# Kernel tuning notes

Measured on AMD Instinct MI355X. Metric: run time of the kernel, lower is better.

## Reference

```python
import jax, jax.numpy as jnp
import numpy as np

N = 100000      # nodes
E = 1600000     # edges
F_IN = 16       # in_features
H = 64          # hidden_channels (heads=1)
E_DIM = 9       # edge_dim
NEG_SLOPE = 0.2


def setup_inputs() -> dict:
    key = jax.random.key(0)
    ks = jax.random.split(key, 11)
    x = jax.random.normal(ks[0], (N, F_IN), jnp.float32)
    edge_index = jax.random.randint(ks[1], (2, E), 0, N, dtype=jnp.int64)
    edge_attr = jax.random.normal(ks[2], (E, E_DIM), jnp.float32)
    s_in = 1.0 / np.sqrt(F_IN)
    s_e = 1.0 / np.sqrt(E_DIM)
    s_h = 1.0 / np.sqrt(H)
    W = jax.random.uniform(ks[3], (F_IN, H), jnp.float32, -s_in, s_in)        # GATConv.lin
    W_edge = jax.random.uniform(ks[4], (E_DIM, H), jnp.float32, -s_e, s_e)    # GATConv.lin_edge
    att_src = jax.random.normal(ks[5], (H,), jnp.float32) * 0.1
    att_dst = jax.random.normal(ks[6], (H,), jnp.float32) * 0.1
    att_edge = jax.random.normal(ks[7], (H,), jnp.float32) * 0.1
    bias = jnp.zeros((H,), jnp.float32)                                        # GATConv bias
    lin_w = jax.random.uniform(ks[8], (H, 1), jnp.float32, -s_h, s_h)          # self.lin
    lin_b = jnp.zeros((1,), jnp.float32)
    return {"x": x, "edge_attr": edge_attr, "W": W, "W_edge": W_edge,
            "att_src": att_src, "att_dst": att_dst, "att_edge": att_edge,
            "bias": bias, "lin_w": lin_w, "lin_b": lin_b, "edge_index": edge_index}


def _gat_forward(x, edge_attr, W, W_edge, att_src, att_dst, att_edge, bias,
                 lin_w, lin_b, edge_index):
    n = x.shape[0]
    src, dst = edge_index[0], edge_index[1]
    h = x @ W                                   # [N, H]
    a_src = h @ att_src                         # [N]
    a_dst = h @ att_dst                         # [N]
    # add_self_loops with fill_value='mean': per-node mean of incoming edge_attr
    ones = jnp.ones((src.shape[0],), x.dtype)
    deg = jax.ops.segment_sum(ones, dst, num_segments=n)
    loop_attr = jax.ops.segment_sum(edge_attr, dst, num_segments=n) / jnp.maximum(deg, 1.0)[:, None]
    loops = jnp.arange(n, dtype=src.dtype)
    src_f = jnp.concatenate([src, loops])       # [E+N]
    dst_f = jnp.concatenate([dst, loops])
    ea_f = jnp.concatenate([edge_attr, loop_attr], axis=0)
    a_edge = (ea_f @ W_edge) @ att_edge         # [E+N]
    alpha = a_src[src_f] + a_dst[dst_f] + a_edge
    alpha = jnp.where(alpha >= 0, alpha, NEG_SLOPE * alpha)  # leaky_relu
    # segment softmax over destination nodes (every node has a self-loop -> no empty segments)
    amax = jax.ops.segment_max(alpha, dst_f, num_segments=n)
    ex = jnp.exp(alpha - amax[dst_f])
    denom = jax.ops.segment_sum(ex, dst_f, num_segments=n)
    alpha = ex / (denom[dst_f] + 1e-16)
    msg = h[src_f] * alpha[:, None]             # [E+N, H]
    out_nodes = jax.ops.segment_sum(msg, dst_f, num_segments=n) + bias
    x2 = jax.nn.relu(out_nodes)
    # edge readout on the ORIGINAL edge list
    pair = (x2[src] + x2[dst]) * 0.5            # [E, H]
    return jax.nn.sigmoid(pair @ lin_w + lin_b) # [E, 1]


def reference(x, edge_attr, W, W_edge, att_src, att_dst, att_edge, bias,
              lin_w, lin_b, edge_index):
    return _gat_forward(x, edge_attr, W, W_edge, att_src, att_dst, att_edge,
                        bias, lin_w, lin_b, edge_index)
```

## Files before the change

kernel.cpp:

```cpp
#include <hip/hip_runtime.h>
#include <hip/hip_bf16.h>
#include <hip/hip_fp16.h>
#include <math.h>

#define N_NODES 100000
#define N_EDGES 1600000
#define F_IN 16
#define HDIM 64
#define E_DIM 9
#define NEG 0.2f

#define CAP 64
#define NSLICE 8
#define SLICE_W 12500
#define SLICE_CAP 210000
#define PART_BLOCKS 1024
#define FIXSCALE 16777216.0f
#define GPAD 64

typedef unsigned long long ull;
typedef long long ll;

__global__ __launch_bounds__(256) void k_node_h(
    const float* __restrict__ x, const float* __restrict__ W,
    const float* __restrict__ att_src, const float* __restrict__ att_dst,
    __hip_bfloat16* __restrict__ hbf, float* __restrict__ a_src,
    float* __restrict__ a_dst) {
  __shared__ float sW[F_IN * HDIM];
  int t = threadIdx.x;
  for (int i = t; i < F_IN * HDIM; i += 256) sW[i] = W[i];
  __syncthreads();
  int lane = t & 63;
  int node = blockIdx.x * 4 + (t >> 6);
  if (node >= N_NODES) return;
  const float* xr = x + node * F_IN;
  float acc = 0.f;
#pragma unroll
  for (int k = 0; k < F_IN; ++k) acc += xr[k] * sW[k * HDIM + lane];
  hbf[(size_t)node * HDIM + lane] = __float2bfloat16(acc);
  float v1 = acc * att_src[lane];
  float v2 = acc * att_dst[lane];
#pragma unroll
  for (int off = 32; off > 0; off >>= 1) {
    v1 += __shfl_down(v1, off);
    v2 += __shfl_down(v2, off);
  }
  if (lane == 0) { a_src[node] = v1; a_dst[node] = v2; }
}

__global__ void k_we(const float* __restrict__ W_edge,
                     const float* __restrict__ att_edge, float* __restrict__ w_e) {
  int d = threadIdx.x;
  if (d < E_DIM) {
    float s = 0.f;
    for (int hh = 0; hh < HDIM; ++hh) s += W_edge[d * HDIM + hh] * att_edge[hh];
    w_e[d] = s;
  }
}

__global__ __launch_bounds__(256) void k_edge_pre(
    const float* __restrict__ ea, const int* __restrict__ ei,
    const float* __restrict__ w_e, const float* __restrict__ a_src,
    const float* __restrict__ a_dst, ull* __restrict__ sstream,
    unsigned* __restrict__ gcount) {
  __shared__ float sea[256 * E_DIM];
  __shared__ float swe[E_DIM];
  __shared__ unsigned wcnt[4][NSLICE];
  __shared__ unsigned woff[4][NSLICE];
  __shared__ unsigned gbase[NSLICE];
  int t = threadIdx.x;
  int wave = t >> 6, lane = t & 63;
  if (t < E_DIM) swe[t] = w_e[t];
  size_t tile = (size_t)blockIdx.x * (256 * E_DIM);
#pragma unroll
  for (int i = 0; i < E_DIM; ++i)
    sea[i * 256 + t] = __builtin_nontemporal_load(ea + tile + i * 256 + t);
  int e = blockIdx.x * 256 + t;
  int s = __builtin_nontemporal_load(ei + e);
  int d = __builtin_nontemporal_load(ei + N_EDGES + e);
  __syncthreads();
  float a_e = 0.f;
#pragma unroll
  for (int k = 0; k < E_DIM; ++k) a_e += sea[t * E_DIM + k] * swe[k];
  float al = a_src[s] + a_dst[d] + a_e;
  al = al >= 0.f ? al : NEG * al;
  float ee = expf(al);
  unsigned b = __float_as_uint(ee);
  b += 0x7fffu + ((b >> 16) & 1u);
  unsigned pk = ((unsigned)s << 15) | ((b >> 16) & 0x7fffu);
  unsigned slice = (unsigned)d / SLICE_W;
  unsigned dloc = (unsigned)d - slice * SLICE_W;
  unsigned aeh = (unsigned)__half_as_ushort(__float2half(a_e));
  ull entry = ((ull)dloc << 48) | ((ull)aeh << 32) | (ull)pk;
  ull lt = (lane == 63) ? 0x7FFFFFFFFFFFFFFFull : ((1ull << lane) - 1ull);
  unsigned myrank = 0;
#pragma unroll
  for (int si = 0; si < NSLICE; ++si) {
    ull m = __ballot(slice == (unsigned)si);
    if (slice == (unsigned)si) myrank = (unsigned)__popcll(m & lt);
    if (lane == 0) wcnt[wave][si] = (unsigned)__popcll(m);
  }
  __syncthreads();
  if (t < NSLICE) {
    unsigned a = 0;
#pragma unroll
    for (int w = 0; w < 4; ++w) { woff[w][t] = a; a += wcnt[w][t]; }
    gbase[t] = atomicAdd(gcount + t * GPAD, a);
  }
  __syncthreads();
  unsigned off = gbase[slice] + woff[wave][slice] + myrank;
  if (off < SLICE_CAP)
    __builtin_nontemporal_store(entry, sstream + (size_t)slice * SLICE_CAP + off);
}

__global__ __launch_bounds__(256) void k_part2(
    const ull* __restrict__ sstream, const unsigned* __restrict__ gcount,
    ull* __restrict__ packed, unsigned* __restrict__ bpack) {
  int t = threadIdx.x;
  int slice = blockIdx.x & (NSLICE - 1);
  int j = blockIdx.x >> 3;
  unsigned n = gcount[slice * GPAD];
  const ull* sp = sstream + (size_t)slice * SLICE_CAP;
  int lo = slice * SLICE_W;
  const unsigned stride = (PART_BLOCKS / NSLICE) * 256;
  for (unsigned i = (unsigned)j * 256 + t; i < n; i += stride) {
    ull entry = sp[i];
    int d = lo + (int)(unsigned)(entry >> 48);
    float ae = __half2float(__ushort_as_half((unsigned short)((entry >> 32) & 0xFFFFu)));
    unsigned pk = (unsigned)(entry & 0xFFFFFFFFu);
    ll q = (ll)lrintf(ae * FIXSCALE);
    ull old = atomicAdd(packed + d, ((ull)q << 20) | 1ull);
    unsigned pos = (unsigned)(old & 0xFFFFFu);
    if (pos < CAP) bpack[(size_t)d * CAP + pos] = pk;
  }
}

__global__ __launch_bounds__(256) void k_gather(
    const ull* __restrict__ packed, const unsigned* __restrict__ bpack,
    const __hip_bfloat16* __restrict__ hbf, const float* __restrict__ a_src,
    const float* __restrict__ a_dst, const float* __restrict__ bias,
    const float* __restrict__ lin_w, float* __restrict__ s_node) {
  int t = threadIdx.x;
  int lane = t & 63;
  int node = blockIdx.x * 4 + (t >> 6);
  if (node >= N_NODES) return;
  ull p = packed[node];
  unsigned deg = (unsigned)(p & 0xFFFFFu);
  float sumae = (float)((double)((ll)p >> 20) * (1.0 / (double)FIXSCALE));
  const unsigned* row = bpack + (size_t)node * CAP;
  float acc = 0.f, denom = 0.f;
  unsigned k = 0;
  for (; k + 8 <= deg; k += 8) {
    uint4 pa = *(const uint4*)(row + k);
    uint4 pb = *(const uint4*)(row + k + 4);
    float e0 = __uint_as_float((pa.x & 0x7fffu) << 16);
    float e1 = __uint_as_float((pa.y & 0x7fffu) << 16);
    float e2 = __uint_as_float((pa.z & 0x7fffu) << 16);
    float e3 = __uint_as_float((pa.w & 0x7fffu) << 16);
    float e4 = __uint_as_float((pb.x & 0x7fffu) << 16);
    float e5 = __uint_as_float((pb.y & 0x7fffu) << 16);
    float e6 = __uint_as_float((pb.z & 0x7fffu) << 16);
    float e7 = __uint_as_float((pb.w & 0x7fffu) << 16);
    float h0 = __bfloat162float(hbf[(size_t)(pa.x >> 15) * HDIM + lane]);
    float h1 = __bfloat162float(hbf[(size_t)(pa.y >> 15) * HDIM + lane]);
    float h2 = __bfloat162float(hbf[(size_t)(pa.z >> 15) * HDIM + lane]);
    float h3 = __bfloat162float(hbf[(size_t)(pa.w >> 15) * HDIM + lane]);
    float h4 = __bfloat162float(hbf[(size_t)(pb.x >> 15) * HDIM + lane]);
    float h5 = __bfloat162float(hbf[(size_t)(pb.y >> 15) * HDIM + lane]);
    float h6 = __bfloat162float(hbf[(size_t)(pb.z >> 15) * HDIM + lane]);
    float h7 = __bfloat162float(hbf[(size_t)(pb.w >> 15) * HDIM + lane]);
    denom += ((e0 + e1) + (e2 + e3)) + ((e4 + e5) + (e6 + e7));
    acc += (e0 * h0 + e1 * h1 + e2 * h2 + e3 * h3)
         + (e4 * h4 + e5 * h5 + e6 * h6 + e7 * h7);
  }
  for (; k + 4 <= deg; k += 4) {
    uint4 p4 = *(const uint4*)(row + k);
    float e0 = __uint_as_float((p4.x & 0x7fffu) << 16);
    float e1 = __uint_as_float((p4.y & 0x7fffu) << 16);
    float e2 = __uint_as_float((p4.z & 0x7fffu) << 16);
    float e3 = __uint_as_float((p4.w & 0x7fffu) << 16);
    float h0 = __bfloat162float(hbf[(size_t)(p4.x >> 15) * HDIM + lane]);
    float h1 = __bfloat162float(hbf[(size_t)(p4.y >> 15) * HDIM + lane]);
    float h2 = __bfloat162float(hbf[(size_t)(p4.z >> 15) * HDIM + lane]);
    float h3 = __bfloat162float(hbf[(size_t)(p4.w >> 15) * HDIM + lane]);
    denom += (e0 + e1) + (e2 + e3);
    acc += e0 * h0 + e1 * h1 + e2 * h2 + e3 * h3;
  }
  for (; k < deg; ++k) {
    unsigned pe = row[k];
    float ee = __uint_as_float((pe & 0x7fffu) << 16);
    denom += ee;
    acc += ee * __bfloat162float(hbf[(size_t)(pe >> 15) * HDIM + lane]);
  }
  float cnt = (float)deg;
  float all = a_src[node] + a_dst[node] + sumae / fmaxf(cnt, 1.f);
  all = all >= 0.f ? all : NEG * all;
  float eel = expf(all);
  denom += eel;
  acc += eel * __bfloat162float(hbf[(size_t)node * HDIM + lane]);
  float o = fmaxf(acc / (denom + 1e-16f) + bias[lane], 0.f) * lin_w[lane];
#pragma unroll
  for (int off = 32; off > 0; off >>= 1) o += __shfl_down(o, off);
  if (lane == 0) s_node[node] = o;
}

__global__ __launch_bounds__(256) void k_out(
    const int* __restrict__ ei, const float* __restrict__ s_node,
    const float* __restrict__ lin_b, float* __restrict__ out) {
  int e = blockIdx.x * 256 + threadIdx.x;
  if (e >= N_EDGES) return;
  int s = __builtin_nontemporal_load(ei + e);
  int d = __builtin_nontemporal_load(ei + N_EDGES + e);
  float z = 0.5f * (s_node[s] + s_node[d]) + lin_b[0];
  float r = 1.f / (1.f + expf(-z));
  __builtin_nontemporal_store(r, out + e);
}

extern "C" void kernel_launch(void* const* d_in, const int* in_sizes, int n_in,
                              void* d_out, int out_size, void* d_ws, size_t ws_size,
                              hipStream_t stream) {
  const float* x        = (const float*)d_in[0];
  const float* edge_attr= (const float*)d_in[1];
  const float* W        = (const float*)d_in[2];
  const float* W_edge   = (const float*)d_in[3];
  const float* att_src  = (const float*)d_in[4];
  const float* att_dst  = (const float*)d_in[5];
  const float* att_edge = (const float*)d_in[6];
  const float* bias     = (const float*)d_in[7];
  const float* lin_w    = (const float*)d_in[8];
  const float* lin_b    = (const float*)d_in[9];
  const int*   ei       = (const int*)d_in[10];
  float* out = (float*)d_out;

  char* base = (char*)d_ws;
  __hip_bfloat16* hbf = (__hip_bfloat16*)base;
  ull* sstream = (ull*)(base + (size_t)N_NODES * HDIM * 2);
  unsigned* bpack = (unsigned*)(sstream + (size_t)NSLICE * SLICE_CAP);
  ull* packed = (ull*)(bpack + (size_t)N_NODES * CAP);
  unsigned* gcount = (unsigned*)(packed + N_NODES);
  float* a_src  = (float*)(gcount + NSLICE * GPAD);
  float* a_dst  = a_src + N_NODES;
  float* s_node = a_dst + N_NODES;
  float* w_e    = s_node + N_NODES;

  hipMemsetAsync(packed, 0,
                 sizeof(ull) * N_NODES + sizeof(unsigned) * NSLICE * GPAD, stream);

  int nb_node   = (N_NODES + 3) / 4;
  int nb_edge_t = N_EDGES / 256;

  k_node_h  <<<nb_node, 256, 0, stream>>>(x, W, att_src, att_dst, hbf, a_src, a_dst);
  k_we      <<<1, 64, 0, stream>>>(W_edge, att_edge, w_e);
  k_edge_pre<<<nb_edge_t, 256, 0, stream>>>(edge_attr, ei, w_e, a_src, a_dst,
                                            sstream, gcount);
  k_part2   <<<PART_BLOCKS, 256, 0, stream>>>(sstream, gcount, packed, bpack);
  k_gather  <<<nb_node, 256, 0, stream>>>(packed, bpack, hbf, a_src, a_dst,
                                          bias, lin_w, s_node);
  k_out     <<<nb_edge_t, 256, 0, stream>>>(ei, s_node, lin_b, out);
}
```

Baseline: 385.7 us.

## Aggregate raw 16-dim inputs instead of projected features, apply W after gather

```diff
diff --git a/kernel.cpp b/kernel.cpp
--- a/kernel.cpp
+++ b/kernel.cpp
@@ -21,10 +21,15 @@
 typedef unsigned long long ull;
 typedef long long ll;
 
+__device__ __forceinline__ void bf2(unsigned u, float& lo, float& hi) {
+  lo = __uint_as_float(u << 16);
+  hi = __uint_as_float(u & 0xFFFF0000u);
+}
+
 __global__ __launch_bounds__(256) void k_node_h(
     const float* __restrict__ x, const float* __restrict__ W,
     const float* __restrict__ att_src, const float* __restrict__ att_dst,
-    __hip_bfloat16* __restrict__ hbf, float* __restrict__ a_src,
+    __hip_bfloat16* __restrict__ xbf, float* __restrict__ a_src,
     float* __restrict__ a_dst) {
   __shared__ float sW[F_IN * HDIM];
   int t = threadIdx.x;
@@ -37,7 +42,7 @@
   float acc = 0.f;
 #pragma unroll
   for (int k = 0; k < F_IN; ++k) acc += xr[k] * sW[k * HDIM + lane];
-  hbf[(size_t)node * HDIM + lane] = __float2bfloat16(acc);
+  if (lane < F_IN) xbf[(size_t)node * F_IN + lane] = __float2bfloat16(xr[lane]);
   float v1 = acc * att_src[lane];
   float v2 = acc * att_dst[lane];
 #pragma unroll
@@ -60,8 +65,7 @@
 
 __global__ __launch_bounds__(256) void k_edge_pre(
     const float* __restrict__ ea, const int* __restrict__ ei,
-    const float* __restrict__ w_e, const float* __restrict__ a_src,
-    const float* __restrict__ a_dst, ull* __restrict__ sstream,
+    const float* __restrict__ w_e, ull* __restrict__ sstream,
     unsigned* __restrict__ gcount) {
   __shared__ float sea[256 * E_DIM];
   __shared__ float swe[E_DIM];
@@ -82,16 +86,10 @@
   float a_e = 0.f;
 #pragma unroll
   for (int k = 0; k < E_DIM; ++k) a_e += sea[t * E_DIM + k] * swe[k];
-  float al = a_src[s] + a_dst[d] + a_e;
-  al = al >= 0.f ? al : NEG * al;
-  float ee = expf(al);
-  unsigned b = __float_as_uint(ee);
-  b += 0x7fffu + ((b >> 16) & 1u);
-  unsigned pk = ((unsigned)s << 15) | ((b >> 16) & 0x7fffu);
   unsigned slice = (unsigned)d / SLICE_W;
   unsigned dloc = (unsigned)d - slice * SLICE_W;
   unsigned aeh = (unsigned)__half_as_ushort(__float2half(a_e));
-  ull entry = ((ull)dloc << 48) | ((ull)aeh << 32) | (ull)pk;
+  ull entry = ((ull)dloc << 48) | ((ull)aeh << 32) | (ull)(unsigned)s;
   ull lt = (lane == 63) ? 0x7FFFFFFFFFFFFFFFull : ((1ull << lane) - 1ull);
   unsigned myrank = 0;
 #pragma unroll
@@ -115,6 +113,7 @@
 
 __global__ __launch_bounds__(256) void k_part2(
     const ull* __restrict__ sstream, const unsigned* __restrict__ gcount,
+    const float* __restrict__ a_src, const float* __restrict__ a_dst,
     ull* __restrict__ packed, unsigned* __restrict__ bpack) {
   int t = threadIdx.x;
   int slice = blockIdx.x & (NSLICE - 1);
@@ -125,9 +124,15 @@
   const unsigned stride = (PART_BLOCKS / NSLICE) * 256;
   for (unsigned i = (unsigned)j * 256 + t; i < n; i += stride) {
     ull entry = sp[i];
+    unsigned src = (unsigned)(entry & 0xFFFFFFFFu);
+    float ae = __half2float(__ushort_as_half((unsigned short)((entry >> 32) & 0xFFFFu)));
     int d = lo + (int)(unsigned)(entry >> 48);
-    float ae = __half2float(__ushort_as_half((unsigned short)((entry >> 32) & 0xFFFFu)));
-    unsigned pk = (unsigned)(entry & 0xFFFFFFFFu);
+    float al = a_src[src] + a_dst[d] + ae;
+    al = al >= 0.f ? al : NEG * al;
+    float ee = expf(al);
+    unsigned b = __float_as_uint(ee);
+    b += 0x7fffu + ((b >> 16) & 1u);
+    unsigned pk = (src << 15) | ((b >> 16) & 0x7fffu);
     ll q = (ll)lrintf(ae * FIXSCALE);
     ull old = atomicAdd(packed + d, ((ull)q << 20) | 1ull);
     unsigned pos = (unsigned)(old & 0xFFFFFu);
@@ -137,71 +142,80 @@
 
 __global__ __launch_bounds__(256) void k_gather(
     const ull* __restrict__ packed, const unsigned* __restrict__ bpack,
-    const __hip_bfloat16* __restrict__ hbf, const float* __restrict__ a_src,
-    const float* __restrict__ a_dst, const float* __restrict__ bias,
-    const float* __restrict__ lin_w, float* __restrict__ s_node) {
-  int t = threadIdx.x;
-  int lane = t & 63;
-  int node = blockIdx.x * 4 + (t >> 6);
+    const __hip_bfloat16* __restrict__ xbf, const float* __restrict__ W,
+    const float* __restrict__ a_src, const float* __restrict__ a_dst,
+    const float* __restrict__ bias, const float* __restrict__ lin_w,
+    float* __restrict__ s_node) {
+  __shared__ float sW[F_IN * HDIM];
+  int t = threadIdx.x;
+  for (int i = t; i < F_IN * HDIM; i += 256) sW[i] = W[i];
+  __syncthreads();
+  int g = t >> 4, i = t & 15;
+  int node = blockIdx.x * 16 + g;
   if (node >= N_NODES) return;
   ull p = packed[node];
   unsigned deg = (unsigned)(p & 0xFFFFFu);
   float sumae = (float)((double)((ll)p >> 20) * (1.0 / (double)FIXSCALE));
+  unsigned degc = deg < CAP ? deg : CAP;
   const unsigned* row = bpack + (size_t)node * CAP;
-  float acc = 0.f, denom = 0.f;
-  unsigned k = 0;
-  for (; k + 8 <= deg; k += 8) {
-    uint4 pa = *(const uint4*)(row + k);
-    uint4 pb = *(const uint4*)(row + k + 4);
-    float e0 = __uint_as_float((pa.x & 0x7fffu) << 16);
-    float e1 = __uint_as_float((pa.y & 0x7fffu) << 16);
-    float e2 = __uint_as_float((pa.z & 0x7fffu) << 16);
-    float e3 = __uint_as_float((pa.w & 0x7fffu) << 16);
-    float e4 = __uint_as_float((pb.x & 0x7fffu) << 16);
-    float e5 = __uint_as_float((pb.y & 0x7fffu) << 16);
-    float e6 = __uint_as_float((pb.z & 0x7fffu) << 16);
-    float e7 = __uint_as_float((pb.w & 0x7fffu) << 16);
-    float h0 = __bfloat162float(hbf[(size_t)(pa.x >> 15) * HDIM + lane]);
-    float h1 = __bfloat162float(hbf[(size_t)(pa.y >> 15) * HDIM + lane]);
-    float h2 = __bfloat162float(hbf[(size_t)(pa.z >> 15) * HDIM + lane]);
-    float h3 = __bfloat162float(hbf[(size_t)(pa.w >> 15) * HDIM + lane]);
-    float h4 = __bfloat162float(hbf[(size_t)(pb.x >> 15) * HDIM + lane]);
-    float h5 = __bfloat162float(hbf[(size_t)(pb.y >> 15) * HDIM + lane]);
-    float h6 = __bfloat162float(hbf[(size_t)(pb.z >> 15) * HDIM + lane]);
-    float h7 = __bfloat162float(hbf[(size_t)(pb.w >> 15) * HDIM + lane]);
-    denom += ((e0 + e1) + (e2 + e3)) + ((e4 + e5) + (e6 + e7));
-    acc += (e0 * h0 + e1 * h1 + e2 * h2 + e3 * h3)
-         + (e4 * h4 + e5 * h5 + e6 * h6 + e7 * h7);
-  }
-  for (; k + 4 <= deg; k += 4) {
-    uint4 p4 = *(const uint4*)(row + k);
-    float e0 = __uint_as_float((p4.x & 0x7fffu) << 16);
-    float e1 = __uint_as_float((p4.y & 0x7fffu) << 16);
-    float e2 = __uint_as_float((p4.z & 0x7fffu) << 16);
-    float e3 = __uint_as_float((p4.w & 0x7fffu) << 16);
-    float h0 = __bfloat162float(hbf[(size_t)(p4.x >> 15) * HDIM + lane]);
-    float h1 = __bfloat162float(hbf[(size_t)(p4.y >> 15) * HDIM + lane]);
-    float h2 = __bfloat162float(hbf[(size_t)(p4.z >> 15) * HDIM + lane]);
-    float h3 = __bfloat162float(hbf[(size_t)(p4.w >> 15) * HDIM + lane]);
-    denom += (e0 + e1) + (e2 + e3);
-    acc += e0 * h0 + e1 * h1 + e2 * h2 + e3 * h3;
-  }
-  for (; k < deg; ++k) {
+  float acc[F_IN];
+#pragma unroll
+  for (int j = 0; j < F_IN; ++j) acc[j] = 0.f;
+  float denom = 0.f;
+  for (unsigned k = i; k < degc; k += 16) {
     unsigned pe = row[k];
     float ee = __uint_as_float((pe & 0x7fffu) << 16);
+    unsigned src = pe >> 15;
+    const uint4* xp = (const uint4*)(xbf + (size_t)src * F_IN);
+    uint4 xa = xp[0], xb = xp[1];
     denom += ee;
-    acc += ee * __bfloat162float(hbf[(size_t)(pe >> 15) * HDIM + lane]);
+    float f0, f1;
+    bf2(xa.x, f0, f1); acc[0] += ee * f0; acc[1] += ee * f1;
+    bf2(xa.y, f0, f1); acc[2] += ee * f0; acc[3] += ee * f1;
+    bf2(xa.z, f0, f1); acc[4] += ee * f0; acc[5] += ee * f1;
+    bf2(xa.w, f0, f1); acc[6] += ee * f0; acc[7] += ee * f1;
+    bf2(xb.x, f0, f1); acc[8] += ee * f0; acc[9] += ee * f1;
+    bf2(xb.y, f0, f1); acc[10] += ee * f0; acc[11] += ee * f1;
+    bf2(xb.z, f0, f1); acc[12] += ee * f0; acc[13] += ee * f1;
+    bf2(xb.w, f0, f1); acc[14] += ee * f0; acc[15] += ee * f1;
+  }
+#pragma unroll
+  for (int off = 8; off > 0; off >>= 1) {
+    denom += __shfl_xor(denom, off, 16);
+#pragma unroll
+    for (int j = 0; j < F_IN; ++j) acc[j] += __shfl_xor(acc[j], off, 16);
   }
   float cnt = (float)deg;
   float all = a_src[node] + a_dst[node] + sumae / fmaxf(cnt, 1.f);
   all = all >= 0.f ? all : NEG * all;
   float eel = expf(all);
   denom += eel;
-  acc += eel * __bfloat162float(hbf[(size_t)node * HDIM + lane]);
-  float o = fmaxf(acc / (denom + 1e-16f) + bias[lane], 0.f) * lin_w[lane];
-#pragma unroll
-  for (int off = 32; off > 0; off >>= 1) o += __shfl_down(o, off);
-  if (lane == 0) s_node[node] = o;
+  {
+    const uint4* xp = (const uint4*)(xbf + (size_t)node * F_IN);
+    uint4 xa = xp[0], xb = xp[1];
+    float f0, f1;
+    bf2(xa.x, f0, f1); acc[0] += eel * f0; acc[1] += eel * f1;
+    bf2(xa.y, f0, f1); acc[2] += eel * f0; acc[3] += eel * f1;
+    bf2(xa.z, f0, f1); acc[4] += eel * f0; acc[5] += eel * f1;
+    bf2(xa.w, f0, f1); acc[6] += eel * f0; acc[7] += eel * f1;
+    bf2(xb.x, f0, f1); acc[8] += eel * f0; acc[9] += eel * f1;
+    bf2(xb.y, f0, f1); acc[10] += eel * f0; acc[11] += eel * f1;
+    bf2(xb.z, f0, f1); acc[12] += eel * f0; acc[13] += eel * f1;
+    bf2(xb.w, f0, f1); acc[14] += eel * f0; acc[15] += eel * f1;
+  }
+  float inv = 1.f / (denom + 1e-16f);
+  float o = 0.f;
+#pragma unroll
+  for (int stp = 0; stp < 4; ++stp) {
+    int h = i + stp * 16;
+    float oh = 0.f;
+#pragma unroll
+    for (int j = 0; j < F_IN; ++j) oh += acc[j] * sW[j * HDIM + h];
+    o += fmaxf(oh * inv + bias[h], 0.f) * lin_w[h];
+  }
+#pragma unroll
+  for (int off = 8; off > 0; off >>= 1) o += __shfl_xor(o, off, 16);
+  if (i == 0) s_node[node] = o;
 }
 
 __global__ __launch_bounds__(256) void k_out(
@@ -233,8 +247,8 @@
   float* out = (float*)d_out;
 
   char* base = (char*)d_ws;
-  __hip_bfloat16* hbf = (__hip_bfloat16*)base;
-  ull* sstream = (ull*)(base + (size_t)N_NODES * HDIM * 2);
+  __hip_bfloat16* xbf = (__hip_bfloat16*)base;
+  ull* sstream = (ull*)(base + (size_t)N_NODES * F_IN * 2);
   unsigned* bpack = (unsigned*)(sstream + (size_t)NSLICE * SLICE_CAP);
   ull* packed = (ull*)(bpack + (size_t)N_NODES * CAP);
   unsigned* gcount = (unsigned*)(packed + N_NODES);
@@ -248,13 +262,14 @@
 
   int nb_node   = (N_NODES + 3) / 4;
   int nb_edge_t = N_EDGES / 256;
-
-  k_node_h  <<<nb_node, 256, 0, stream>>>(x, W, att_src, att_dst, hbf, a_src, a_dst);
+  int nb_gather = (N_NODES + 15) / 16;
+
+  k_node_h  <<<nb_node, 256, 0, stream>>>(x, W, att_src, att_dst, xbf, a_src, a_dst);
   k_we      <<<1, 64, 0, stream>>>(W_edge, att_edge, w_e);
-  k_edge_pre<<<nb_edge_t, 256, 0, stream>>>(edge_attr, ei, w_e, a_src, a_dst,
-                                            sstream, gcount);
-  k_part2   <<<PART_BLOCKS, 256, 0, stream>>>(sstream, gcount, packed, bpack);
-  k_gather  <<<nb_node, 256, 0, stream>>>(packed, bpack, hbf, a_src, a_dst,
-                                          bias, lin_w, s_node);
+  k_edge_pre<<<nb_edge_t, 256, 0, stream>>>(edge_attr, ei, w_e, sstream, gcount);
+  k_part2   <<<PART_BLOCKS, 256, 0, stream>>>(sstream, gcount, a_src, a_dst,
+                                              packed, bpack);
+  k_gather  <<<nb_gather, 256, 0, stream>>>(packed, bpack, xbf, W, a_src, a_dst,
+                                            bias, lin_w, s_node);
   k_out     <<<nb_edge_t, 256, 0, stream>>>(ei, s_node, lin_b, out);
 }
```

Result: faster. 363.0 us (-5.9%).
